# Kernel optimization log

Measured on AMD Instinct MI355X. Metric: run time of the kernel, lower is better.

## Reference

```python
import jax, jax.numpy as jnp
import numpy as np

N0, N1, N2 = 200000, 25000, 5000
FANOUT = 16
IN_FEATS, N_HIDDEN, N_CLASSES = 500, 128, 47


def setup_inputs() -> dict:
    key = jax.random.key(0)
    ks = jax.random.split(key, 7)
    features = jax.random.normal(ks[0], (N0, IN_FEATS), dtype=jnp.float32)
    src0 = jax.random.randint(ks[1], (N1, FANOUT), 0, N0)  # neighbors of layer-1 nodes
    src1 = jax.random.randint(ks[2], (N2, FANOUT), 0, N1)  # neighbors of seed nodes
    W1 = jax.random.normal(ks[3], (IN_FEATS, N_HIDDEN), dtype=jnp.float32) * 0.05
    b1 = jnp.zeros((N_HIDDEN,), dtype=jnp.float32)
    W2 = jax.random.normal(ks[4], (2 * N_HIDDEN, N_CLASSES), dtype=jnp.float32) * 0.05
    b2 = jnp.zeros((N_CLASSES,), dtype=jnp.float32)
    return {"features": features, "src0": src0, "src1": src1,
            "W1": W1, "b1": b1, "W2": W2, "b2": b2}


def reference(features, src0, src1, W1, b1, W2, b2):
    # Block 0: copy_src + mailbox mean over fixed fanout, then Linear + concat(h, relu(h))
    m0 = features[src0].mean(axis=1)            # [N1, IN_FEATS]
    h1 = m0 @ W1 + b1                            # [N1, N_HIDDEN]
    h1 = jnp.concatenate([h1, jax.nn.relu(h1)], axis=1)  # [N1, 2*N_HIDDEN] (skip_start concat)
    # Block 1: mean aggregation + output Linear (no activation)
    m1 = h1[src1].mean(axis=1)                   # [N2, 2*N_HIDDEN]
    out = m1 @ W2 + b2                           # [N2, N_CLASSES]
    return out
```

## Files before the change

kernel.cpp:

```cpp
#include <hip/hip_runtime.h>

#define N0        200000
#define N1        25000
#define N2        5000
#define FANOUT    16
#define IN_FEATS  500
#define NH        128
#define NC        47
#define K_PAD     512
#define TILE_R    16
#define NTILES    (N0 / TILE_R)
#define GRID_A    512

typedef __attribute__((ext_vector_type(4))) float f32x4;
typedef __attribute__((ext_vector_type(8))) short bf16x8;
typedef __attribute__((ext_vector_type(2))) unsigned int uint2_;
typedef __attribute__((ext_vector_type(4))) unsigned int uint4_;
typedef __attribute__((ext_vector_type(4))) int int4_;

__device__ __forceinline__ unsigned short f2bf(float f) {
    unsigned int u = __builtin_bit_cast(unsigned int, f);
    u += 0x7fffu + ((u >> 16) & 1u);
    return (unsigned short)(u >> 16);
}
__device__ __forceinline__ float bfhi(unsigned int u) {
    return __builtin_bit_cast(float, u & 0xffff0000u);
}
__device__ __forceinline__ float bflo(unsigned int u) {
    return __builtin_bit_cast(float, u << 16);
}

__global__ __launch_bounds__(256) void k0_transpose(
    const float* __restrict__ W1, unsigned short* __restrict__ Wt)
{
    __shared__ unsigned short sm[64][NH];
    const int t = threadIdx.x;
    const int kbase = blockIdx.x * 64;

    for (int r = t >> 7; r < 64; r += 2) {
        const int k = kbase + r;
        const int c = t & (NH - 1);
        sm[r][c] = f2bf(k < IN_FEATS ? W1[(size_t)k * NH + c] : 0.f);
    }
    __syncthreads();

    const int c  = t >> 1;
    const int ko = (t & 1) * 32;
    unsigned short* dst = Wt + (size_t)c * K_PAD + kbase + ko;
    #pragma unroll
    for (int i = 0; i < 32; i += 8) {
        bf16x8 v;
        #pragma unroll
        for (int e = 0; e < 8; ++e) v[e] = (short)sm[ko + i + e][c];
        *(bf16x8*)(dst + i) = v;
    }
}

__global__ __launch_bounds__(512, 4) void kA_gemm(
    const float* __restrict__ features,
    const unsigned short* __restrict__ Wt,
    unsigned short* __restrict__ H0)
{
    __shared__ unsigned short A[2][TILE_R * K_PAD];

    const int tid  = threadIdx.x;
    const int lane = tid & 63;
    const int wv   = tid >> 6;
    const int l15  = lane & 15;
    const int lq   = lane >> 4;

    bf16x8 bfrag[16];
    {
        const unsigned short* bp = Wt + (size_t)(wv * 16 + l15) * K_PAD + lq * 8;
        #pragma unroll
        for (int kk = 0; kk < 16; ++kk)
            bfrag[kk] = *(const bf16x8*)(bp + kk * 32);
    }

    if (tid < 96) {
        const int b  = tid / 48, rem = tid % 48;
        const int r  = rem / 3,  j   = rem % 3;
        const int k4 = 500 + j * 4;
        uint2_ z = {0u, 0u};
        *(uint2_*)((char*)&A[b][0] + r * 1024 + ((k4 * 2) ^ ((r & 7) << 4))) = z;
    }

    f32x4 ld[4];
    int cur = 0;
    int t = blockIdx.x;

    {
        const f32x4* slab = (const f32x4*)(features + (size_t)t * TILE_R * IN_FEATS);
        #pragma unroll
        for (int i = 0; i < 3; ++i) ld[i] = __builtin_nontemporal_load(slab + tid + 512 * i);
        if (tid < 464) ld[3] = __builtin_nontemporal_load(slab + tid + 1536);
        #pragma unroll
        for (int i = 0; i < 4; ++i) {
            if (i < 3 || tid < 464) {
                const int c  = tid + 512 * i;
                const int r  = c / 125;
                const int k4 = (c - r * 125) * 4;
                uint2_ w;
                w.x = (unsigned int)f2bf(ld[i].x) | ((unsigned int)f2bf(ld[i].y) << 16);
                w.y = (unsigned int)f2bf(ld[i].z) | ((unsigned int)f2bf(ld[i].w) << 16);
                *(uint2_*)((char*)&A[0][0] + r * 1024 + ((k4 * 2) ^ ((r & 7) << 4))) = w;
            }
        }
    }
    __syncthreads();

    while (t < NTILES) {
        const int tn = t + GRID_A;

        if (tn < NTILES) {
            const f32x4* slab = (const f32x4*)(features + (size_t)tn * TILE_R * IN_FEATS);
            #pragma unroll
            for (int i = 0; i < 3; ++i) ld[i] = __builtin_nontemporal_load(slab + tid + 512 * i);
            if (tid < 464) ld[3] = __builtin_nontemporal_load(slab + tid + 1536);
        }

        f32x4 acc = (f32x4){0.f, 0.f, 0.f, 0.f};
        const char* base = (const char*)&A[cur][0];
        const int abase = l15 * 1024;
        const int sw    = (l15 & 7) << 4;

        #pragma unroll
        for (int kk = 0; kk < 16; ++kk) {
            const int ke = kk * 32 + lq * 8;
            bf16x8 a = *(const bf16x8*)(base + abase + ((ke * 2) ^ sw));
            acc = __builtin_amdgcn_mfma_f32_16x16x32_bf16(a, bfrag[kk], acc, 0, 0, 0);
        }

        const int rowb = t * TILE_R;
        const int col  = wv * 16 + l15;
        #pragma unroll
        for (int rr = 0; rr < 4; ++rr) {
            H0[(size_t)(rowb + lq * 4 + rr) * NH + col] = f2bf(acc[rr]);
        }

        if (tn < NTILES) {
            char* nb = (char*)&A[cur ^ 1][0];
            #pragma unroll
            for (int i = 0; i < 4; ++i) {
                if (i < 3 || tid < 464) {
                    const int c  = tid + 512 * i;
                    const int r  = c / 125;
                    const int k4 = (c - r * 125) * 4;
                    uint2_ w;
                    w.x = (unsigned int)f2bf(ld[i].x) | ((unsigned int)f2bf(ld[i].y) << 16);
                    w.y = (unsigned int)f2bf(ld[i].z) | ((unsigned int)f2bf(ld[i].w) << 16);
                    *(uint2_*)(nb + r * 1024 + ((k4 * 2) ^ ((r & 7) << 4))) = w;
                }
            }
        }

        __syncthreads();
        cur ^= 1;
        t = tn;
    }
}

__global__ __launch_bounds__(256, 8) void kB_gather(
    const unsigned short* __restrict__ H0,
    const int*   __restrict__ src0,
    const float* __restrict__ b1,
    unsigned short* __restrict__ h1cat)
{
    const int lane = threadIdx.x & 63;
    const int wv   = threadIdx.x >> 6;
    const int row  = blockIdx.x * 4 + wv;
    const int c16  = lane >> 2;
    const int jq   = lane & 3;

    int4_ nb4 = *(const int4_*)(src0 + row * FANOUT + jq * 4);

    const size_t c8 = (size_t)c16 * 8;
    float acc[8] = {0.f,0.f,0.f,0.f,0.f,0.f,0.f,0.f};

    uint4_ v0 = *(const uint4_*)(H0 + (size_t)nb4.x * NH + c8);
    uint4_ v1 = *(const uint4_*)(H0 + (size_t)nb4.y * NH + c8);
    uint4_ v2 = *(const uint4_*)(H0 + (size_t)nb4.z * NH + c8);
    uint4_ v3 = *(const uint4_*)(H0 + (size_t)nb4.w * NH + c8);

    acc[0] += bflo(v0.x); acc[1] += bfhi(v0.x); acc[2] += bflo(v0.y); acc[3] += bfhi(v0.y);
    acc[4] += bflo(v0.z); acc[5] += bfhi(v0.z); acc[6] += bflo(v0.w); acc[7] += bfhi(v0.w);
    acc[0] += bflo(v1.x); acc[1] += bfhi(v1.x); acc[2] += bflo(v1.y); acc[3] += bfhi(v1.y);
    acc[4] += bflo(v1.z); acc[5] += bfhi(v1.z); acc[6] += bflo(v1.w); acc[7] += bfhi(v1.w);
    acc[0] += bflo(v2.x); acc[1] += bfhi(v2.x); acc[2] += bflo(v2.y); acc[3] += bfhi(v2.y);
    acc[4] += bflo(v2.z); acc[5] += bfhi(v2.z); acc[6] += bflo(v2.w); acc[7] += bfhi(v2.w);
    acc[0] += bflo(v3.x); acc[1] += bfhi(v3.x); acc[2] += bflo(v3.y); acc[3] += bfhi(v3.y);
    acc[4] += bflo(v3.z); acc[5] += bfhi(v3.z); acc[6] += bflo(v3.w); acc[7] += bfhi(v3.w);

    #pragma unroll
    for (int e = 0; e < 8; ++e) {
        float a = acc[e];
        a += __shfl_xor(a, 1);
        a += __shfl_xor(a, 2);
        acc[e] = a;
    }

    f32x4 b_lo = *(const f32x4*)(b1 + c8);
    f32x4 b_hi = *(const f32x4*)(b1 + c8 + 4);
    float h[8];
    h[0] = acc[0]*0.0625f + b_lo.x; h[1] = acc[1]*0.0625f + b_lo.y;
    h[2] = acc[2]*0.0625f + b_lo.z; h[3] = acc[3]*0.0625f + b_lo.w;
    h[4] = acc[4]*0.0625f + b_hi.x; h[5] = acc[5]*0.0625f + b_hi.y;
    h[6] = acc[6]*0.0625f + b_hi.z; h[7] = acc[7]*0.0625f + b_hi.w;

    unsigned short* dst = h1cat + (size_t)row * 256;
    if (jq == 0) {
        uint4_ w;
        w.x = (unsigned int)f2bf(h[0]) | ((unsigned int)f2bf(h[1]) << 16);
        w.y = (unsigned int)f2bf(h[2]) | ((unsigned int)f2bf(h[3]) << 16);
        w.z = (unsigned int)f2bf(h[4]) | ((unsigned int)f2bf(h[5]) << 16);
        w.w = (unsigned int)f2bf(h[6]) | ((unsigned int)f2bf(h[7]) << 16);
        *(uint4_*)(dst + c8) = w;
    } else if (jq == 1) {
        uint4_ w;
        w.x = (unsigned int)f2bf(h[0]>0.f?h[0]:0.f) | ((unsigned int)f2bf(h[1]>0.f?h[1]:0.f) << 16);
        w.y = (unsigned int)f2bf(h[2]>0.f?h[2]:0.f) | ((unsigned int)f2bf(h[3]>0.f?h[3]:0.f) << 16);
        w.z = (unsigned int)f2bf(h[4]>0.f?h[4]:0.f) | ((unsigned int)f2bf(h[5]>0.f?h[5]:0.f) << 16);
        w.w = (unsigned int)f2bf(h[6]>0.f?h[6]:0.f) | ((unsigned int)f2bf(h[7]>0.f?h[7]:0.f) << 16);
        *(uint4_*)(dst + NH + c8) = w;
    }
}

__global__ __launch_bounds__(256) void k2_fused(
    const unsigned short* __restrict__ h1cat,
    const int*   __restrict__ src1,
    const float* __restrict__ W2,
    const float* __restrict__ b2,
    float*       __restrict__ out)
{
    __shared__ float sm[8][256];

    const int tid = threadIdx.x;
    const int r   = tid >> 5;
    const int s   = tid & 31;
    const int row = blockIdx.x * 8 + r;

    float acc[8] = {0.f,0.f,0.f,0.f,0.f,0.f,0.f,0.f};
    #pragma unroll
    for (int j = 0; j < FANOUT; ++j) {
        const int nb = src1[row * FANOUT + j];
        uint4_ v = *(const uint4_*)(h1cat + (size_t)nb * 256 + s * 8);
        acc[0] += bflo(v.x); acc[1] += bfhi(v.x);
        acc[2] += bflo(v.y); acc[3] += bfhi(v.y);
        acc[4] += bflo(v.z); acc[5] += bfhi(v.z);
        acc[6] += bflo(v.w); acc[7] += bfhi(v.w);
    }
    #pragma unroll
    for (int e = 0; e < 8; ++e) sm[r][s * 8 + e] = acc[e] * 0.0625f;
    __syncthreads();

    const int c0 = s, c1 = s + 32;
    float o0 = b2[c0];
    float o1 = (c1 < NC) ? b2[c1] : 0.f;
    for (int k = 0; k < 256; k += 4) {
        f32x4 mv = *(const f32x4*)&sm[r][k];
        #pragma unroll
        for (int e = 0; e < 4; ++e) {
            const float* wrow = W2 + (size_t)(k + e) * NC;
            o0 += mv[e] * wrow[c0];
            if (c1 < NC) o1 += mv[e] * wrow[c1];
        }
    }
    out[(size_t)row * NC + c0] = o0;
    if (c1 < NC) out[(size_t)row * NC + c1] = o1;
}

extern "C" void kernel_launch(void* const* d_in, const int* in_sizes, int n_in,
                              void* d_out, int out_size, void* d_ws, size_t ws_size,
                              hipStream_t stream)
{
    const float* features = (const float*)d_in[0];
    const int*   src0     = (const int*)  d_in[1];
    const int*   src1     = (const int*)  d_in[2];
    const float* W1       = (const float*)d_in[3];
    const float* b1       = (const float*)d_in[4];
    const float* W2       = (const float*)d_in[5];
    const float* b2       = (const float*)d_in[6];
    float*       out      = (float*)d_out;

    unsigned short* Wt    = (unsigned short*)d_ws;
    unsigned short* H0    = Wt + (size_t)NH * K_PAD;
    unsigned short* h1cat = H0 + (size_t)N0 * NH;

    hipLaunchKernelGGL(k0_transpose, dim3(K_PAD / 64), dim3(256), 0, stream, W1, Wt);
    hipLaunchKernelGGL(kA_gemm,   dim3(GRID_A),        dim3(512), 0, stream, features, Wt, H0);
    hipLaunchKernelGGL(kB_gather, dim3(N1 / 4),        dim3(256), 0, stream, H0, src0, b1, h1cat);
    hipLaunchKernelGGL(k2_fused,  dim3(N2 / 8),        dim3(256), 0, stream, h1cat, src1, W2, b2, out);
}
```

Before: 182.2 us.

## Stage GEMM output through LDS and reorder block-1 as GEMM-then-gather

kA now writes each tile's bf16 output into a double-buffered LDS tile and stores it as coalesced 16-byte rows during the next iteration, replacing scattered 2-byte global stores. Block 1 is restructured to apply W2 to all N1 rows first, then gather and average the 47-wide results per seed node. This shrinks gather width from 256 to 47 but multiplies the small GEMM work by N1/N2. It adds LDS use and an extra kernel launch.

Result: slower. 209.7 us (+15.1%).

```diff
diff --git a/kernel.cpp b/kernel.cpp
--- a/kernel.cpp
+++ b/kernel.cpp
@@ -62,6 +62,7 @@
     unsigned short* __restrict__ H0)
 {
     __shared__ unsigned short A[2][TILE_R * K_PAD];
+    __shared__ unsigned short OT[2][TILE_R][136];
 
     const int tid  = threadIdx.x;
     const int lane = tid & 63;
@@ -88,6 +89,8 @@
     f32x4 ld[4];
     int cur = 0;
     int t = blockIdx.x;
+    int pend_rowb = -1;
+    int pcur = 0;
 
     {
         const f32x4* slab = (const f32x4*)(features + (size_t)t * TILE_R * IN_FEATS);
@@ -119,6 +122,13 @@
             if (tid < 464) ld[3] = __builtin_nontemporal_load(slab + tid + 1536);
         }
 
+        if (pend_rowb >= 0 && tid < 256) {
+            const int r = tid >> 4;
+            const int c = (tid & 15) * 8;
+            bf16x8 v = *(const bf16x8*)&OT[pcur][r][c];
+            *(bf16x8*)(H0 + (size_t)(pend_rowb + r) * NH + c) = v;
+        }
+
         f32x4 acc = (f32x4){0.f, 0.f, 0.f, 0.f};
         const char* base = (const char*)&A[cur][0];
         const int abase = l15 * 1024;
@@ -131,12 +141,9 @@
             acc = __builtin_amdgcn_mfma_f32_16x16x32_bf16(a, bfrag[kk], acc, 0, 0, 0);
         }
 
-        const int rowb = t * TILE_R;
-        const int col  = wv * 16 + l15;
-        #pragma unroll
-        for (int rr = 0; rr < 4; ++rr) {
-            H0[(size_t)(rowb + lq * 4 + rr) * NH + col] = f2bf(acc[rr]);
-        }
+        #pragma unroll
+        for (int rr = 0; rr < 4; ++rr)
+            OT[cur][lq * 4 + rr][wv * 16 + l15] = f2bf(acc[rr]);
 
         if (tn < NTILES) {
             char* nb = (char*)&A[cur ^ 1][0];
@@ -155,8 +162,17 @@
         }
 
         __syncthreads();
+        pend_rowb = t * TILE_R;
+        pcur = cur;
         cur ^= 1;
         t = tn;
+    }
+
+    if (pend_rowb >= 0 && tid < 256) {
+        const int r = tid >> 4;
+        const int c = (tid & 15) * 8;
+        bf16x8 v = *(const bf16x8*)&OT[pcur][r][c];
+        *(bf16x8*)(H0 + (size_t)(pend_rowb + r) * NH + c) = v;
     }
 }
 
@@ -225,32 +241,25 @@
     }
 }
 
-__global__ __launch_bounds__(256) void k2_fused(
+__global__ __launch_bounds__(256) void kG_gemm(
     const unsigned short* __restrict__ h1cat,
-    const int*   __restrict__ src1,
     const float* __restrict__ W2,
     const float* __restrict__ b2,
-    float*       __restrict__ out)
+    float*       __restrict__ G)
 {
     __shared__ float sm[8][256];
 
-    const int tid = threadIdx.x;
-    const int r   = tid >> 5;
-    const int s   = tid & 31;
-    const int row = blockIdx.x * 8 + r;
-
-    float acc[8] = {0.f,0.f,0.f,0.f,0.f,0.f,0.f,0.f};
-    #pragma unroll
-    for (int j = 0; j < FANOUT; ++j) {
-        const int nb = src1[row * FANOUT + j];
-        uint4_ v = *(const uint4_*)(h1cat + (size_t)nb * 256 + s * 8);
-        acc[0] += bflo(v.x); acc[1] += bfhi(v.x);
-        acc[2] += bflo(v.y); acc[3] += bfhi(v.y);
-        acc[4] += bflo(v.z); acc[5] += bfhi(v.z);
-        acc[6] += bflo(v.w); acc[7] += bfhi(v.w);
-    }
-    #pragma unroll
-    for (int e = 0; e < 8; ++e) sm[r][s * 8 + e] = acc[e] * 0.0625f;
+    const int tid  = threadIdx.x;
+    const int row0 = blockIdx.x * 8;
+    const int r    = tid >> 5;
+    const int s    = tid & 31;
+
+    {
+        uint4_ v = *(const uint4_*)(h1cat + (size_t)(row0 + r) * 256 + s * 8);
+        float* d = &sm[r][s * 8];
+        d[0]=bflo(v.x); d[1]=bfhi(v.x); d[2]=bflo(v.y); d[3]=bfhi(v.y);
+        d[4]=bflo(v.z); d[5]=bfhi(v.z); d[6]=bflo(v.w); d[7]=bfhi(v.w);
+    }
     __syncthreads();
 
     const int c0 = s, c1 = s + 32;
@@ -265,8 +274,29 @@
             if (c1 < NC) o1 += mv[e] * wrow[c1];
         }
     }
-    out[(size_t)row * NC + c0] = o0;
-    if (c1 < NC) out[(size_t)row * NC + c1] = o1;
+    G[(size_t)(row0 + r) * NC + c0] = o0;
+    if (c1 < NC) G[(size_t)(row0 + r) * NC + c1] = o1;
+}
+
+__global__ __launch_bounds__(256, 8) void k2_gather(
+    const float* __restrict__ G,
+    const int*   __restrict__ src1,
+    float*       __restrict__ out)
+{
+    const int lane = threadIdx.x & 63;
+    const int wv   = threadIdx.x >> 6;
+    const int row  = blockIdx.x * 4 + wv;
+    const int rb   = row * FANOUT;
+
+    if (lane < NC) {
+        float acc = 0.f;
+        #pragma unroll
+        for (int j = 0; j < FANOUT; ++j) {
+            const int nb = src1[rb + j];
+            acc += G[(size_t)nb * NC + lane];
+        }
+        out[(size_t)row * NC + lane] = acc * 0.0625f;
+    }
 }
 
 extern "C" void kernel_launch(void* const* d_in, const int* in_sizes, int n_in,
@@ -285,9 +315,11 @@
     unsigned short* Wt    = (unsigned short*)d_ws;
     unsigned short* H0    = Wt + (size_t)NH * K_PAD;
     unsigned short* h1cat = H0 + (size_t)N0 * NH;
+    float*          G     = (float*)(h1cat + (size_t)N1 * 256);
 
     hipLaunchKernelGGL(k0_transpose, dim3(K_PAD / 64), dim3(256), 0, stream, W1, Wt);
     hipLaunchKernelGGL(kA_gemm,   dim3(GRID_A),        dim3(512), 0, stream, features, Wt, H0);
     hipLaunchKernelGGL(kB_gather, dim3(N1 / 4),        dim3(256), 0, stream, H0, src0, b1, h1cat);
-    hipLaunchKernelGGL(k2_fused,  dim3(N2 / 8),        dim3(256), 0, stream, h1cat, src1, W2, b2, out);
-}
+    hipLaunchKernelGGL(kG_gemm,   dim3(N1 / 8),        dim3(256), 0, stream, h1cat, W2, b2, G);
+    hipLaunchKernelGGL(k2_gather, dim3(N2 / 4),        dim3(256), 0, stream, G, src1, out);
+}
```
